# Kernel optimization log

Hardware: AMD Instinct MI355X
Metric: run time of the kernel (lower is better)

Reference implementation:

```python
import jax, jax.numpy as jnp
import numpy as np

SHAPES = ((64, 64), (32, 32), (16, 16), (8, 8))
LEVEL_STARTS = np.concatenate([[0], np.cumsum([h * w for h, w in SHAPES])]).tolist()
N_LEVELS = 4; N_HEADS = 8; N_POINTS = 4; D_MODEL = 256; HEAD_DIM = 32; D_FFN = 1024; NUM_LAYERS = 2
LEN_IN = sum(h * w for h, w in SHAPES)
BATCH = 2


def setup_inputs():
    key = jax.random.key(0)
    ks = iter(jax.random.split(key, 40))
    r = lambda shape, s=1.0: jax.random.normal(next(ks), shape, dtype=jnp.float32) * s
    L = NUM_LAYERS
    return {
        "src": r((BATCH, LEN_IN, D_MODEL)),
        "pos": r((BATCH, LEN_IN, D_MODEL), 0.5),
        "valid_ratios": jnp.ones((BATCH, N_LEVELS, 2), jnp.float32),
        "Wv": r((L, D_MODEL, D_MODEL), 0.05), "bv": jnp.zeros((L, D_MODEL), jnp.float32),
        "Woff": r((L, D_MODEL, N_HEADS * N_LEVELS * N_POINTS * 2), 0.002),
        "boff": r((L, N_HEADS * N_LEVELS * N_POINTS * 2), 0.5),
        "Wa": r((L, D_MODEL, N_HEADS * N_LEVELS * N_POINTS), 0.05),
        "ba": jnp.zeros((L, N_HEADS * N_LEVELS * N_POINTS), jnp.float32),
        "Wo": r((L, D_MODEL, D_MODEL), 0.05), "bo": jnp.zeros((L, D_MODEL), jnp.float32),
        "g1": jnp.ones((L, D_MODEL), jnp.float32), "be1": jnp.zeros((L, D_MODEL), jnp.float32),
        "Wl1": r((L, D_MODEL, D_FFN), 0.05), "bl1": jnp.zeros((L, D_FFN), jnp.float32),
        "Wl2": r((L, D_FFN, D_MODEL), 0.05), "bl2": jnp.zeros((L, D_MODEL), jnp.float32),
        "g2": jnp.ones((L, D_MODEL), jnp.float32), "be2": jnp.zeros((L, D_MODEL), jnp.float32),
    }


def layer_norm(x, g, b, eps=1e-5):
    m = jnp.mean(x, -1, keepdims=True)
    v = jnp.mean(jnp.square(x - m), -1, keepdims=True)
    return (x - m) * jax.lax.rsqrt(v + eps) * g + b


def make_reference_points(valid_ratios):
    # DeformableTransformerEncoder.get_reference_points, vectorized per level
    refs = []
    for lvl, (H, W) in enumerate(SHAPES):
        gy, gx = jnp.meshgrid(jnp.arange(H, dtype=jnp.float32) + 0.5,
                              jnp.arange(W, dtype=jnp.float32) + 0.5, indexing="ij")
        ry = gy.reshape(-1)[None] / (valid_ratios[:, lvl, 1][:, None] * H)
        rx = gx.reshape(-1)[None] / (valid_ratios[:, lvl, 0][:, None] * W)
        refs.append(jnp.stack([rx, ry], -1))  # [N, H*W, 2]
    ref = jnp.concatenate(refs, 1)  # [N, Len, 2]
    return ref[:, :, None, :] * valid_ratios[:, None]  # [N, Len, n_levels, 2]


def ms_deform_attn(query, input_flatten, reference_points, Wv, bv, Woff, boff, Wa, ba, Wo, bo):
    N, Lq, _ = query.shape
    value = (input_flatten @ Wv + bv).reshape(N, -1, N_HEADS, HEAD_DIM)
    off = (query @ Woff + boff).reshape(N, Lq, N_HEADS, N_LEVELS, N_POINTS, 2)
    aw = (query @ Wa + ba).reshape(N, Lq, N_HEADS, N_LEVELS * N_POINTS)
    aw = jax.nn.softmax(aw, -1).reshape(N, Lq, N_HEADS, N_LEVELS, N_POINTS)
    # normalizer is (W, H) per level, as in MSDeformAttn
    normalizer = jnp.array([[w, h] for h, w in SHAPES], jnp.float32)
    loc = reference_points[:, :, None, :, None, :] + off / normalizer[None, None, None, :, None, :]
    acc = jnp.zeros((N, N_HEADS, Lq, HEAD_DIM), query.dtype)
    for lvl, (H, W) in enumerate(SHAPES):
        s = LEVEL_STARTS[lvl]
        val = value[:, s:s + H * W].transpose(0, 2, 1, 3)  # [N, heads, H*W, hd]
        # grid_sample bilinear, align_corners=False, zero padding
        x = loc[:, :, :, lvl, :, 0] * W - 0.5  # [N, Lq, heads, P]
        y = loc[:, :, :, lvl, :, 1] * H - 0.5
        x0 = jnp.floor(x); y0 = jnp.floor(y)
        wx1 = x - x0; wy1 = y - y0
        ix0 = x0.astype(jnp.int32); iy0 = y0.astype(jnp.int32)

        def corner(ix, iy, w):
            valid = (ix >= 0) & (ix < W) & (iy >= 0) & (iy < H)
            idx = jnp.clip(iy, 0, H - 1) * W + jnp.clip(ix, 0, W - 1)
            idx = idx.transpose(0, 2, 1, 3).reshape(N, N_HEADS, Lq * N_POINTS)
            g = jnp.take_along_axis(val, idx[..., None], axis=2).reshape(N, N_HEADS, Lq, N_POINTS, HEAD_DIM)
            w = jnp.where(valid, w, 0.0).transpose(0, 2, 1, 3)  # [N, heads, Lq, P]
            return g * w[..., None]

        sampled = (corner(ix0, iy0, (1 - wx1) * (1 - wy1))
                   + corner(ix0 + 1, iy0, wx1 * (1 - wy1))
                   + corner(ix0, iy0 + 1, (1 - wx1) * wy1)
                   + corner(ix0 + 1, iy0 + 1, wx1 * wy1))
        acc = acc + (sampled * aw[:, :, :, lvl].transpose(0, 2, 1, 3)[..., None]).sum(3)
    out = acc.transpose(0, 2, 1, 3).reshape(N, Lq, D_MODEL)
    return out @ Wo + bo


def reference(src, pos, valid_ratios, Wv, bv, Woff, boff, Wa, ba, Wo, bo,
              g1, be1, Wl1, bl1, Wl2, bl2, g2, be2):
    ref_pts = make_reference_points(valid_ratios)
    out = src
    for l in range(NUM_LAYERS):
        q = out + pos  # with_pos_embed
        attn = ms_deform_attn(q, out, ref_pts, Wv[l], bv[l], Woff[l], boff[l],
                              Wa[l], ba[l], Wo[l], bo[l])
        out = layer_norm(out + attn, g1[l], be1[l])
        ffn = jax.nn.relu(out @ Wl1[l] + bl1[l]) @ Wl2[l] + bl2[l]
        out = layer_norm(out + ffn, g2[l], be2[l])
    return out
```

## Files before the change

### kernel.cpp

```cpp
#include <hip/hip_runtime.h>
#include <math.h>

#define LEN   5440
#define NB    2
#define MROWS (NB * LEN)
#define DM    256
#define NH    8
#define HD    32
#define NLV   4
#define NPT   4
#define DFFN  1024

typedef __attribute__((ext_vector_type(8))) short bf16x8;
typedef __attribute__((ext_vector_type(4))) short bf16x4;
typedef __attribute__((ext_vector_type(4))) float f32x4;

#define MFMA16 __builtin_amdgcn_mfma_f32_16x16x32_bf16

__device__ __forceinline__ short f2bf(float f) {
    union { float f; unsigned u; } cv; cv.f = f;
    unsigned r = cv.u + 0x7fffu + ((cv.u >> 16) & 1u);
    return (short)(r >> 16);
}
__device__ __forceinline__ float bf2f(short s) {
    union { unsigned u; float f; } cv;
    cv.u = ((unsigned)(unsigned short)s) << 16;
    return cv.f;
}

__device__ __forceinline__ void gload16(const short* g, short* l) {
    __builtin_amdgcn_global_load_lds(
        (__attribute__((address_space(1))) void*)g,
        (__attribute__((address_space(3))) void*)l, 16, 0, 0);
}

template <int N> __device__ __forceinline__ void vmwait();
template <> __device__ __forceinline__ void vmwait<0>() { asm volatile("s_waitcnt vmcnt(0)" ::: "memory"); }
template <> __device__ __forceinline__ void vmwait<4>() { asm volatile("s_waitcnt vmcnt(4)" ::: "memory"); }
template <> __device__ __forceinline__ void vmwait<5>() { asm volatile("s_waitcnt vmcnt(5)" ::: "memory"); }

__device__ __forceinline__ int swz(int row) { return (row >> 1) & 3; }

__global__ __launch_bounds__(256) void prep_all(
    const float* __restrict__ Wv,  const float* __restrict__ Woff,
    const float* __restrict__ Wa,  const float* __restrict__ Wo,
    const float* __restrict__ Wl1, const float* __restrict__ Wl2,
    short* __restrict__ out,
    const float4* __restrict__ s4, const float4* __restrict__ p4,
    bf16x4* __restrict__ curb, bf16x4* __restrict__ qb)
{
    __shared__ short T[32][33];
    if (blockIdx.x >= 1472) {
        const int i = (blockIdx.x - 1472) * 256 + threadIdx.x;
        float4 s = s4[i], p = p4[i];
        bf16x4 c, q;
        c[0] = f2bf(s.x); c[1] = f2bf(s.y); c[2] = f2bf(s.z); c[3] = f2bf(s.w);
        q[0] = f2bf(s.x + p.x); q[1] = f2bf(s.y + p.y);
        q[2] = f2bf(s.z + p.z); q[3] = f2bf(s.w + p.w);
        curb[i] = c; qb[i] = q;
        return;
    }
    int bx = blockIdx.x;
    int l  = bx / 736;
    int t  = bx % 736;
    const float* src; int K, N; long doff;
    if      (t < 64)  { src = Wv;   K = 256;  N = 256;  doff = 0;      }
    else if (t < 128) { src = Woff; K = 256;  N = 256;  doff = 65536;  t -= 64;  }
    else if (t < 160) { src = Wa;   K = 256;  N = 128;  doff = 131072; t -= 128; }
    else if (t < 224) { src = Wo;   K = 256;  N = 256;  doff = 163840; t -= 160; }
    else if (t < 480) { src = Wl1;  K = 256;  N = 1024; doff = 229376; t -= 224; }
    else              { src = Wl2;  K = 1024; N = 256;  doff = 491520; t -= 480; }
    src += (long)l * K * N;
    short* dst = out + (long)l * 753664 + doff;

    const int ntx = N / 32;
    const int n0 = (t % ntx) * 32, k0 = (t / ntx) * 32;

    const int tid = threadIdx.x;
    {
        const int n = tid & 31, kq = tid >> 5;
        #pragma unroll
        for (int i = 0; i < 4; ++i) {
            int k = kq * 4 + i;
            T[n][k] = f2bf(src[(long)(k0 + k) * N + n0 + n]);
        }
    }
    __syncthreads();
    {
        const int k = tid & 31, nq = tid >> 5;
        #pragma unroll
        for (int i = 0; i < 4; ++i) {
            int n = nq * 4 + i;
            dst[(long)(n0 + n) * K + k0 + k] = T[n][k];
        }
    }
}

template <int RELU, int OMODE, int K>
__device__ __forceinline__ void gemm_core128_v2(
    short* As, short* Bs,
    const short* __restrict__ A, const short* __restrict__ Wt,
    const float* __restrict__ bias, float* __restrict__ Cf,
    short* __restrict__ Cb, int ldc, int m0, int wrow0, int ccol0)
{
    constexpr int NT = K / 32;
    static_assert(NT >= 4 && (NT & 1) == 0, "NT even >= 4");
    const int t    = threadIdx.x;
    const int wave = t >> 6, lane = t & 63;
    const int wm   = (wave & 1) * 64;
    const int wn   = (wave >> 1) * 64;
    const int lm   = lane & 15;
    const int chkg = lane >> 4;

    const short* aS[2]; const short* bS[2];
    short *aD[2], *bD[2];
    #pragma unroll
    for (int i = 0; i < 2; ++i) {
        const int c   = wave * 2 + i;
        const int row = c * 16 + (lane >> 2);
        const int xc  = (lane & 3) ^ swz(row);
        aS[i] = A  + (long)(m0 + row) * K + xc * 8;
        bS[i] = Wt + (long)(wrow0 + row) * K + xc * 8;
        aD[i] = As + c * 512;
        bD[i] = Bs + c * 512;
    }

    int offA[4], offB[4];
    #pragma unroll
    for (int s = 0; s < 4; ++s) {
        const int r = wm + s * 16 + lm;
        offA[s] = r * 32 + (chkg ^ swz(r)) * 8;
    }
    #pragma unroll
    for (int u = 0; u < 4; ++u) {
        const int r = wn + u * 16 + lm;
        offB[u] = r * 32 + (chkg ^ swz(r)) * 8;
    }

    f32x4 acc[4][4] = {};

#define STG128(BUF, KT) do {                                          \
        const int _ko = (KT) * 32;                                    \
        gload16(aS[0] + _ko, aD[0] + (BUF) * 4096);                   \
        gload16(bS[0] + _ko, bD[0] + (BUF) * 4096);                   \
        gload16(aS[1] + _ko, aD[1] + (BUF) * 4096);                   \
        gload16(bS[1] + _ko, bD[1] + (BUF) * 4096);                   \
    } while (0)

#define GB128(T, BUF, WN, DOSTAGE) do {                               \
        vmwait<WN>();                                                 \
        __builtin_amdgcn_s_barrier();                                 \
        bf16x8 af[4], bv[4];                                          \
        _Pragma("unroll")                                             \
        for (int s = 0; s < 4; ++s)                                   \
            af[s] = *(const bf16x8*)(As + (BUF) * 4096 + offA[s]);    \
        _Pragma("unroll")                                             \
        for (int u = 0; u < 4; ++u)                                   \
            bv[u] = *(const bf16x8*)(Bs + (BUF) * 4096 + offB[u]);    \
        asm volatile("s_waitcnt lgkmcnt(0)" ::: "memory");            \
        __builtin_amdgcn_s_barrier();                                 \
        __builtin_amdgcn_sched_barrier(0);                            \
        if (DOSTAGE) STG128(BUF, (T) + 2);                            \
        _Pragma("unroll")                                             \
        for (int s = 0; s < 4; ++s)                                   \
            _Pragma("unroll")                                         \
            for (int u = 0; u < 4; ++u)                               \
                acc[s][u] = MFMA16(af[s], bv[u], acc[s][u], 0, 0, 0); \
    } while (0)

    STG128(0, 0);
    STG128(1, 1);
    for (int tt = 0; tt < NT - 2; tt += 2) {
        GB128(tt,     0, 4, true);
        GB128(tt + 1, 1, 4, true);
    }
    GB128(NT - 2, 0, 4, false);
    GB128(NT - 1, 1, 0, false);
#undef GB128
#undef STG128

    const int col = lane & 15;
    const int rq  = (lane >> 4) * 4;
    #pragma unroll
    for (int s = 0; s < 4; ++s) {
        #pragma unroll
        for (int u = 0; u < 4; ++u) {
            const int gn = ccol0 + wn + u * 16 + col;
            const float bb = bias[gn];
            #pragma unroll
            for (int r = 0; r < 4; ++r) {
                const int gm = m0 + wm + s * 16 + rq + r;
                float v = acc[s][u][r] + bb;
                if (RELU) v = fmaxf(v, 0.f);
                if (OMODE == 0) {
                    Cf[(long)gm * ldc + gn] = v;
                } else if (OMODE == 1) {
                    Cb[(long)gm * ldc + gn] = f2bf(v);
                } else {
                    const int n   = gm / LEN;
                    const int pix = gm - n * LEN;
                    const int h   = gn >> 5, d = gn & 31;
                    Cb[((long)(n * NH + h) * LEN + pix) * 32 + d] = f2bf(v);
                }
            }
        }
    }
}

template <int RELU, int OMODE, int K>
__global__ __launch_bounds__(256) void gemm128v2(
    const short* __restrict__ A, const short* __restrict__ Wt,
    const float* __restrict__ bias, float* Cf, short* Cb, int ldc)
{
    __shared__ __align__(16) short As[2 * 128 * 32];
    __shared__ __align__(16) short Bs[2 * 128 * 32];
    gemm_core128_v2<RELU, OMODE, K>(As, Bs, A, Wt, bias, Cf, Cb, ldc,
                                    blockIdx.y * 128, blockIdx.x * 128,
                                    blockIdx.x * 128);
}

__global__ __launch_bounds__(256) void gemm_qkv128(
    const short* __restrict__ curb, const short* __restrict__ qb,
    const short* __restrict__ Wt, const float* __restrict__ bv,
    const float* __restrict__ boff, const float* __restrict__ ba,
    short* __restrict__ Vb, float* __restrict__ OFF, float* __restrict__ AW)
{
    __shared__ __align__(16) short As[2 * 128 * 32];
    __shared__ __align__(16) short Bs[2 * 128 * 32];
    const int n0 = blockIdx.x * 128;
    if (n0 < 256) {
        gemm_core128_v2<0, 2, 256>(As, Bs, curb, Wt, bv, (float*)nullptr, Vb,
                                   256, blockIdx.y * 128, n0, n0);
    } else if (n0 < 512) {
        gemm_core128_v2<0, 0, 256>(As, Bs, qb, Wt, boff, OFF, (short*)nullptr,
                                   256, blockIdx.y * 128, n0, n0 - 256);
    } else {
        gemm_core128_v2<0, 0, 256>(As, Bs, qb, Wt, ba, AW, (short*)nullptr,
                                   128, blockIdx.y * 128, n0, n0 - 512);
    }
}

template <int K>
__global__ __launch_bounds__(256) void gemm_ln(
    const short* __restrict__ A, const short* __restrict__ Wt,
    const float* __restrict__ bias, const short* __restrict__ residb,
    const float* __restrict__ g, const float* __restrict__ be,
    short* __restrict__ outb, short* __restrict__ outq,
    float* __restrict__ outf, const float* __restrict__ pos)
{
    constexpr int NT = K / 32;
    __shared__ __align__(16) short As[2 * 32 * 32];
    __shared__ __align__(16) short Bs[2 * 256 * 32];
    __shared__ float red[2][32][2];

    const int t    = threadIdx.x;
    const int wave = t >> 6, lane = t & 63;
    const int wm   = (wave & 1) * 16;
    const int wn   = (wave >> 1) * 128;
    const int lm   = lane & 15;
    const int chkg = lane >> 4;
    const int rq   = chkg * 4;
    const int m0   = blockIdx.x * 32;
    const bool hasA = (wave & 1) == 0;

    short rr[8][4];
    #pragma unroll
    for (int u = 0; u < 8; ++u)
        #pragma unroll
        for (int r = 0; r < 4; ++r)
            rr[u][r] = residb[(long)(m0 + wm + rq + r) * DM + wn + u * 16 + lm];
    asm volatile("" ::: "memory");

    const short* bSp[4]; short* bDp[4];
    #pragma unroll
    for (int i = 0; i < 4; ++i) {
        const int c   = wave * 4 + i;
        const int row = c * 16 + (lane >> 2);
        const int xc  = (lane & 3) ^ swz(row);
        bSp[i] = Wt + (long)row * K + xc * 8;
        bDp[i] = Bs + c * 512;
    }
    const short* aSp = nullptr; short* aDp = nullptr;
    if (hasA) {
        const int c   = wave >> 1;
        const int row = c * 16 + (lane >> 2);
        const int xc  = (lane & 3) ^ swz(row);
        aSp = A + (long)(m0 + row) * K + xc * 8;
        aDp = As + c * 512;
    }

    const int offA = (wm + lm) * 32 + (chkg ^ swz(wm + lm)) * 8;
    int offB[8];
    #pragma unroll
    for (int u = 0; u < 8; ++u) {
        const int r = wn + u * 16 + lm;
        offB[u] = r * 32 + (chkg ^ swz(r)) * 8;
    }

    f32x4 acc[8] = {};

#define STGL(BUF, KT) do {                                            \
        const int _ko = (KT) * 32;                                    \
        if (hasA) gload16(aSp + _ko, aDp + (BUF) * 1024);             \
        gload16(bSp[0] + _ko, bDp[0] + (BUF) * 8192);                 \
        gload16(bSp[1] + _ko, bDp[1] + (BUF) * 8192);                 \
        gload16(bSp[2] + _ko, bDp[2] + (BUF) * 8192);                 \
        gload16(bSp[3] + _ko, bDp[3] + (BUF) * 8192);                 \
    } while (0)

#define GBLN(T, BUF, WA, WB, DOSTAGE) do {                            \
        if (hasA) vmwait<WA>(); else vmwait<WB>();                    \
        __builtin_amdgcn_s_barrier();                                 \
        bf16x8 af = *(const bf16x8*)(As + (BUF) * 1024 + offA);       \
        bf16x8 bv[8];                                                 \
        _Pragma("unroll")                                             \
        for (int u = 0; u < 8; ++u)                                   \
            bv[u] = *(const bf16x8*)(Bs + (BUF) * 8192 + offB[u]);    \
        asm volatile("s_waitcnt lgkmcnt(0)" ::: "memory");            \
        __builtin_amdgcn_s_barrier();                                 \
        __builtin_amdgcn_sched_barrier(0);                            \
        if (DOSTAGE) STGL(BUF, (T) + 2);                              \
        _Pragma("unroll")                                             \
        for (int u = 0; u < 8; ++u)                                   \
            acc[u] = MFMA16(af, bv[u], acc[u], 0, 0, 0);              \
    } while (0)

    STGL(0, 0);
    STGL(1, 1);
    for (int tt = 0; tt < NT - 2; tt += 2) {
        GBLN(tt,     0, 5, 4, true);
        GBLN(tt + 1, 1, 5, 4, true);
    }
    GBLN(NT - 2, 0, 5, 4, false);
    GBLN(NT - 1, 1, 0, 0, false);
#undef GBLN
#undef STGL

    #pragma unroll
    for (int u = 0; u < 8; ++u) {
        const int gn = wn + u * 16 + lm;
        const float bb = bias[gn];
        #pragma unroll
        for (int r = 0; r < 4; ++r)
            acc[u][r] += bb + bf2f(rr[u][r]);
    }

    float rs[4], r2[4];
    #pragma unroll
    for (int r = 0; r < 4; ++r) {
        float s = 0.f, s2 = 0.f;
        #pragma unroll
        for (int u = 0; u < 8; ++u) { const float v = acc[u][r]; s += v; s2 += v * v; }
        rs[r] = s; r2[r] = s2;
    }
    #pragma unroll
    for (int o = 1; o < 16; o <<= 1)
        #pragma unroll
        for (int r = 0; r < 4; ++r) {
            rs[r] += __shfl_xor(rs[r], o, 64);
            r2[r] += __shfl_xor(r2[r], o, 64);
        }
    if (lm == 0) {
        #pragma unroll
        for (int r = 0; r < 4; ++r) {
            red[wave >> 1][wm + rq + r][0] = rs[r];
            red[wave >> 1][wm + rq + r][1] = r2[r];
        }
    }
    __syncthreads();
    #pragma unroll
    for (int r = 0; r < 4; ++r) {
        const int row = wm + rq + r;
        const float ts = red[0][row][0] + red[1][row][0];
        const float t2 = red[0][row][1] + red[1][row][1];
        const float mean = ts * (1.f / DM);
        const float var  = t2 * (1.f / DM) - mean * mean;
        rs[r] = mean;
        r2[r] = rsqrtf(var + 1e-5f);
    }
    #pragma unroll
    for (int u = 0; u < 8; ++u) {
        const int gn = wn + u * 16 + lm;
        const float gg = g[gn], bbe = be[gn];
        #pragma unroll
        for (int r = 0; r < 4; ++r) {
            const long gm = m0 + wm + rq + r;
            const float o = (acc[u][r] - rs[r]) * r2[r] * gg + bbe;
            if (outb) outb[gm * DM + gn] = f2bf(o);
            if (outq) outq[gm * DM + gn] = f2bf(o + pos[gm * DM + gn]);
            if (outf) outf[gm * DM + gn] = o;
        }
    }
}

template <int KLEN, int KSTR>
__global__ __launch_bounds__(256) void ln2_part_k(
    const short* __restrict__ A0, const short* __restrict__ Wt0,
    float* __restrict__ PART)
{
    constexpr int NT = KLEN / 32;
    static_assert(NT >= 4 && (NT & 1) == 0, "NT even >= 4");
    __shared__ __align__(16) short As[2 * 32 * 32];
    __shared__ __align__(16) short Bs[2 * 256 * 32];

    const int kk = blockIdx.x;
    const int m0 = blockIdx.y * 32;
    const short* A  = A0  + kk * KLEN;
    const short* Wt = Wt0 + kk * KLEN;
    float* Pout = PART + (long)kk * MROWS * DM;

    const int t    = threadIdx.x;
    const int wave = t >> 6, lane = t & 63;
    const int wm   = (wave & 1) * 16;
    const int wn   = (wave >> 1) * 128;
    const int lm   = lane & 15;
    const int chkg = lane >> 4;
    const int rq   = chkg * 4;
    const bool hasA = (wave & 1) == 0;

    const short* bSp[4]; short* bDp[4];
    #pragma unroll
    for (int i = 0; i < 4; ++i) {
        const int c   = wave * 4 + i;
        const int row = c * 16 + (lane >> 2);
        const int xc  = (lane & 3) ^ swz(row);
        bSp[i] = Wt + (long)row * KSTR + xc * 8;
        bDp[i] = Bs + c * 512;
    }
    const short* aSp = nullptr; short* aDp = nullptr;
    if (hasA) {
        const int c   = wave >> 1;
        const int row = c * 16 + (lane >> 2);
        const int xc  = (lane & 3) ^ swz(row);
        aSp = A + (long)(m0 + row) * KSTR + xc * 8;
        aDp = As + c * 512;
    }

    const int offA = (wm + lm) * 32 + (chkg ^ swz(wm + lm)) * 8;
    int offB[8];
    #pragma unroll
    for (int u = 0; u < 8; ++u) {
        const int r = wn + u * 16 + lm;
        offB[u] = r * 32 + (chkg ^ swz(r)) * 8;
    }

    f32x4 acc[8] = {};

#define STGP(BUF, KT) do {                                            \
        const int _ko = (KT) * 32;                                    \
        if (hasA) gload16(aSp + _ko, aDp + (BUF) * 1024);             \
        gload16(bSp[0] + _ko, bDp[0] + (BUF) * 8192);                 \
        gload16(bSp[1] + _ko, bDp[1] + (BUF) * 8192);                 \
        gload16(bSp[2] + _ko, bDp[2] + (BUF) * 8192);                 \
        gload16(bSp[3] + _ko, bDp[3] + (BUF) * 8192);                 \
    } while (0)

#define GBP(T, BUF, WA, WB, DOSTAGE) do {                             \
        if (hasA) vmwait<WA>(); else vmwait<WB>();                    \
        __builtin_amdgcn_s_barrier();                                 \
        bf16x8 af = *(const bf16x8*)(As + (BUF) * 1024 + offA);       \
        bf16x8 bv[8];                                                 \
        _Pragma("unroll")                                             \
        for (int u = 0; u < 8; ++u)                                   \
            bv[u] = *(const bf16x8*)(Bs + (BUF) * 8192 + offB[u]);    \
        asm volatile("s_waitcnt lgkmcnt(0)" ::: "memory");            \
        __builtin_amdgcn_s_barrier();                                 \
        __builtin_amdgcn_sched_barrier(0);                            \
        if (DOSTAGE) STGP(BUF, (T) + 2);                              \
        _Pragma("unroll")                                             \
        for (int u = 0; u < 8; ++u)                                   \
            acc[u] = MFMA16(af, bv[u], acc[u], 0, 0, 0);              \
    } while (0)

    STGP(0, 0);
    STGP(1, 1);
    for (int tt = 0; tt < NT - 2; tt += 2) {
        GBP(tt,     0, 5, 4, true);
        GBP(tt + 1, 1, 5, 4, true);
    }
    GBP(NT - 2, 0, 5, 4, false);
    GBP(NT - 1, 1, 0, 0, false);
#undef GBP
#undef STGP

    #pragma unroll
    for (int u = 0; u < 8; ++u) {
        const int gn = wn + u * 16 + lm;
        #pragma unroll
        for (int r = 0; r < 4; ++r)
            Pout[(long)(m0 + wm + rq + r) * DM + gn] = acc[u][r];
    }
}

__global__ __launch_bounds__(256) void ln2_fin_k(
    const float* __restrict__ PART, const short* __restrict__ residb,
    const float* __restrict__ bl2, const float* __restrict__ g,
    const float* __restrict__ be, short* __restrict__ outb,
    short* __restrict__ outq, float* __restrict__ outf,
    const float* __restrict__ pos)
{
    const int wave = threadIdx.x >> 6, lane = threadIdx.x & 63;
    const int c0 = lane * 4;
    const f32x4 bb = *(const f32x4*)(bl2 + c0);
    const f32x4 gg = *(const f32x4*)(g + c0);
    const f32x4 ee = *(const f32x4*)(be + c0);
    #pragma unroll 1
    for (int r = 0; r < 8; ++r) {
        const long row = (long)blockIdx.x * 32 + wave * 8 + r;
        const f32x4 p0 = *(const f32x4*)(PART + row * DM + c0);
        const f32x4 p1 = *(const f32x4*)(PART + (long)MROWS * DM + row * DM + c0);
        const bf16x4 rr = *(const bf16x4*)(residb + row * DM + c0);
        float v[4]; float s = 0.f, s2 = 0.f;
        #pragma unroll
        for (int j = 0; j < 4; ++j) {
            v[j] = p0[j] + p1[j] + bb[j] + bf2f(rr[j]);
            s += v[j]; s2 += v[j] * v[j];
        }
        #pragma unroll
        for (int o = 1; o < 64; o <<= 1) {
            s  += __shfl_xor(s,  o, 64);
            s2 += __shfl_xor(s2, o, 64);
        }
        const float mean = s * (1.f / DM);
        const float var  = s2 * (1.f / DM) - mean * mean;
        const float rstd = rsqrtf(var + 1e-5f);
        float o4[4];
        #pragma unroll
        for (int j = 0; j < 4; ++j)
            o4[j] = (v[j] - mean) * rstd * gg[j] + ee[j];
        if (outb) {
            bf16x4 ob;
            #pragma unroll
            for (int j = 0; j < 4; ++j) ob[j] = f2bf(o4[j]);
            *(bf16x4*)(outb + row * DM + c0) = ob;
        }
        if (outq) {
            const f32x4 pp = *(const f32x4*)(pos + row * DM + c0);
            bf16x4 oq;
            #pragma unroll
            for (int j = 0; j < 4; ++j) oq[j] = f2bf(o4[j] + pp[j]);
            *(bf16x4*)(outq + row * DM + c0) = oq;
        }
        if (outf) {
            f32x4 of;
            #pragma unroll
            for (int j = 0; j < 4; ++j) of[j] = o4[j];
            *(f32x4*)(outf + row * DM + c0) = of;
        }
    }
}

__global__ __launch_bounds__(256) void deform_attn_v3(
    const short* __restrict__ Vb,
    const float* __restrict__ OFF,
    const float* __restrict__ AW,
    const float* __restrict__ vr,
    bf16x4* __restrict__ ATTb)
{
    const int starts[5] = {0, 4096, 5120, 5376, 5440};
    const int dims[4]   = {64, 32, 16, 8};

    const int wave = threadIdx.x >> 6;
    const int lane = threadIdx.x & 63;
    const int h    = lane >> 3;
    const int d4   = lane & 7;

    const int gq = blockIdx.x * 4 + wave;
    const int n  = gq / LEN;
    const int q  = gq % LEN;

    int lq = 3;
    if (q < 4096) lq = 0; else if (q < 5120) lq = 1; else if (q < 5376) lq = 2;
    const int r  = q - starts[lq];
    const int Wq = dims[lq];
    const int gy = r / Wq, gx = r % Wq;
    const float vrxq = vr[(n * NLV + lq) * 2 + 0];
    const float vryq = vr[(n * NLV + lq) * 2 + 1];
    const float rx = (gx + 0.5f) / (vrxq * Wq);
    const float ry = (gy + 0.5f) / (vryq * Wq);

    const long row = (long)n * LEN + q;

    const float* awp = AW + row * 128 + h * 16;
    float a[16];
    float mx = -1e30f;
    #pragma unroll
    for (int i = 0; i < 16; ++i) { a[i] = awp[i]; mx = fmaxf(mx, a[i]); }
    float s = 0.f;
    #pragma unroll
    for (int i = 0; i < 16; ++i) { a[i] = __expf(a[i] - mx); s += a[i]; }
    const float inv = 1.f / s;

    const float* offp = OFF + row * 256 + h * 32;

    float4 acc = {0.f, 0.f, 0.f, 0.f};
    #pragma unroll
    for (int lvl = 0; lvl < NLV; ++lvl) {
        const int Hl = dims[lvl];
        const int Wl = Hl;
        const float fW = (float)Wl;
        const int sb = starts[lvl];
        const float lx = rx * vr[(n * NLV + lvl) * 2 + 0];
        const float ly = ry * vr[(n * NLV + lvl) * 2 + 1];
        const short* vb = Vb + ((long)(n * NH + h) * LEN + sb) * 32 + d4 * 4;
        #pragma unroll
        for (int p = 0; p < NPT; ++p) {
            const float ox = offp[lvl * 8 + p * 2 + 0];
            const float oy = offp[lvl * 8 + p * 2 + 1];
            const float x = fmaf(lx, fW, ox) - 0.5f;
            const float y = fmaf(ly, fW, oy) - 0.5f;
            const float x0f = floorf(x), y0f = floorf(y);
            const int ix0 = (int)x0f, iy0 = (int)y0f;
            const float wx1 = x - x0f, wy1 = y - y0f;
            const float wx0 = 1.f - wx1, wy0 = 1.f - wy1;

            const bool vx0 = (ix0 >= 0)     && (ix0 < Wl);
            const bool vx1 = (ix0 + 1 >= 0) && (ix0 + 1 < Wl);
            const bool vy0 = (iy0 >= 0)     && (iy0 < Hl);
            const bool vy1 = (iy0 + 1 >= 0) && (iy0 + 1 < Hl);
            const int cx0 = min(max(ix0, 0), Wl - 1);
            const int cx1 = min(max(ix0 + 1, 0), Wl - 1);
            const int cy0 = min(max(iy0, 0), Hl - 1);
            const int cy1 = min(max(iy0 + 1, 0), Hl - 1);

            const float w00 = (vx0 && vy0) ? wx0 * wy0 : 0.f;
            const float w10 = (vx1 && vy0) ? wx1 * wy0 : 0.f;
            const float w01 = (vx0 && vy1) ? wx0 * wy1 : 0.f;
            const float w11 = (vx1 && vy1) ? wx1 * wy1 : 0.f;

            const bf16x4 g00 = *(const bf16x4*)(vb + (long)(cy0 * Wl + cx0) * 32);
            const bf16x4 g10 = *(const bf16x4*)(vb + (long)(cy0 * Wl + cx1) * 32);
            const bf16x4 g01 = *(const bf16x4*)(vb + (long)(cy1 * Wl + cx0) * 32);
            const bf16x4 g11 = *(const bf16x4*)(vb + (long)(cy1 * Wl + cx1) * 32);

            const float awv = a[lvl * 4 + p] * inv;
            #pragma unroll
            for (int e = 0; e < 4; ++e) {
                float sv = w00 * bf2f(g00[e]) + w10 * bf2f(g10[e])
                         + w01 * bf2f(g01[e]) + w11 * bf2f(g11[e]);
                (&acc.x)[e] += awv * sv;
            }
        }
    }
    bf16x4 ob;
    ob[0] = f2bf(acc.x); ob[1] = f2bf(acc.y);
    ob[2] = f2bf(acc.z); ob[3] = f2bf(acc.w);
    ATTb[row * 64 + h * 8 + d4] = ob;
}

extern "C" void kernel_launch(void* const* d_in, const int* in_sizes, int n_in,
                              void* d_out, int out_size, void* d_ws, size_t ws_size,
                              hipStream_t stream)
{
    const float* src = (const float*)d_in[0];
    const float* pos = (const float*)d_in[1];
    const float* vr  = (const float*)d_in[2];
    const float* Wv_   = (const float*)d_in[3];
    const float* bv_   = (const float*)d_in[4];
    const float* Woff_ = (const float*)d_in[5];
    const float* boff_ = (const float*)d_in[6];
    const float* Wa_   = (const float*)d_in[7];
    const float* ba_   = (const float*)d_in[8];
    const float* Wo_   = (const float*)d_in[9];
    const float* bo_   = (const float*)d_in[10];
    const float* g1_   = (const float*)d_in[11];
    const float* be1_  = (const float*)d_in[12];
    const float* Wl1_  = (const float*)d_in[13];
    const float* bl1_  = (const float*)d_in[14];
    const float* Wl2_  = (const float*)d_in[15];
    const float* bl2_  = (const float*)d_in[16];
    const float* g2_   = (const float*)d_in[17];
    const float* be2_  = (const float*)d_in[18];

    const long SZ = (long)MROWS * DM;
    float* ws = (float*)d_ws;
    float* OFF  = ws;
    float* AW   = OFF + SZ;
    short* Vb   = (short*)(AW + (long)MROWS * 128);
    short* curb = Vb   + SZ;
    short* qb   = curb + SZ;
    short* ATTb = qb   + SZ;
    short* XAb  = ATTb + SZ;
    short* FFNb = XAb  + SZ;
    short* Wt   = FFNb + (long)MROWS * DFFN;
    float* PART = (float*)(Wt + 2L * 753664);

    const dim3 blk(256);
    const int GYM = MROWS / 128;
    const int GLN = MROWS / 32;

    hipLaunchKernelGGL(prep_all, dim3(1472 + SZ / 4 / 256), blk, 0, stream,
                       Wv_, Woff_, Wa_, Wo_, Wl1_, Wl2_, Wt,
                       (const float4*)src, (const float4*)pos,
                       (bf16x4*)curb, (bf16x4*)qb);

    for (int l = 0; l < 2; ++l) {
        const short* Wbase = Wt + (long)l * 753664;
        const float* bv   = bv_   + (long)l * DM;
        const float* boff = boff_ + (long)l * 256;
        const float* ba   = ba_   + (long)l * 128;
        const float* bo   = bo_   + (long)l * DM;
        const float* g1   = g1_   + (long)l * DM;
        const float* be1  = be1_  + (long)l * DM;
        const float* bl1  = bl1_  + (long)l * DFFN;
        const float* bl2  = bl2_  + (long)l * DM;
        const float* g2   = g2_   + (long)l * DM;
        const float* be2  = be2_  + (long)l * DM;

        hipLaunchKernelGGL(gemm_qkv128, dim3(5, GYM), blk, 0, stream,
                           curb, qb, Wbase, bv, boff, ba, Vb, OFF, AW);
        hipLaunchKernelGGL(deform_attn_v3, dim3(MROWS / 4), blk, 0, stream,
                           Vb, OFF, AW, vr, (bf16x4*)ATTb);
        hipLaunchKernelGGL((gemm_ln<256>), dim3(GLN), blk, 0, stream,
                           ATTb, Wbase + 163840, bo, curb, g1, be1,
                           XAb, (short*)nullptr, (float*)nullptr,
                           (const float*)nullptr);
        hipLaunchKernelGGL((gemm128v2<1, 1, 256>), dim3(8, GYM), blk, 0, stream,
                           XAb, Wbase + 229376, bl1, (float*)nullptr, FFNb, 1024);
        hipLaunchKernelGGL((ln2_part_k<512, 1024>), dim3(2, GLN), blk, 0, stream,
                           FFNb, Wbase + 491520, PART);
        if (l == 0) {
            hipLaunchKernelGGL(ln2_fin_k, dim3(GLN), blk, 0, stream,
                               PART, XAb, bl2, g2, be2,
                               curb, qb, (float*)nullptr, pos);
        } else {
            hipLaunchKernelGGL(ln2_fin_k, dim3(GLN), blk, 0, stream,
                               PART, XAb, bl2, g2, be2,
                               (short*)nullptr, (short*)nullptr,
                               (float*)d_out, (const float*)nullptr);
        }
    }
}
```

Baseline: 293.8 us.

## Double GEMM K-tile depth to 64 with 8-way XOR swizzled LDS layout

All bf16 MFMA GEMM kernels (QKV, FFN1, output-proj+LN, FFN2 partial) now stage 64-wide K tiles instead of 32, halving the number of barrier/wait iterations and issuing two MFMAs per fragment per step. The LDS layout changes to 64-element rows with a row&7 XOR swizzle, and the per-wave load distribution is reworked so all waves load A uniformly. LDS use doubles per block (up to ~72KB for the LN kernels), which may reduce occupancy; the static_assert NT>=4 now requires K>=256, which the K=256 GEMMs exactly meet.

```diff
diff --git a/kernel.cpp b/kernel.cpp
--- a/kernel.cpp
+++ b/kernel.cpp
@@ -36,10 +36,9 @@
 
 template <int N> __device__ __forceinline__ void vmwait();
 template <> __device__ __forceinline__ void vmwait<0>() { asm volatile("s_waitcnt vmcnt(0)" ::: "memory"); }
-template <> __device__ __forceinline__ void vmwait<4>() { asm volatile("s_waitcnt vmcnt(4)" ::: "memory"); }
-template <> __device__ __forceinline__ void vmwait<5>() { asm volatile("s_waitcnt vmcnt(5)" ::: "memory"); }
-
-__device__ __forceinline__ int swz(int row) { return (row >> 1) & 3; }
+template <> __device__ __forceinline__ void vmwait<8>() { asm volatile("s_waitcnt vmcnt(8)" ::: "memory"); }
+template <> __device__ __forceinline__ void vmwait<9>() { asm volatile("s_waitcnt vmcnt(9)" ::: "memory"); }
+
 
 __global__ __launch_bounds__(256) void prep_all(
     const float* __restrict__ Wv,  const float* __restrict__ Woff,
@@ -97,13 +96,13 @@
 }
 
 template <int RELU, int OMODE, int K>
-__device__ __forceinline__ void gemm_core128_v2(
+__device__ __forceinline__ void gemm_core128_v3(
     short* As, short* Bs,
     const short* __restrict__ A, const short* __restrict__ Wt,
     const float* __restrict__ bias, float* __restrict__ Cf,
     short* __restrict__ Cb, int ldc, int m0, int wrow0, int ccol0)
 {
-    constexpr int NT = K / 32;
+    constexpr int NT = K / 64;
     static_assert(NT >= 4 && (NT & 1) == 0, "NT even >= 4");
     const int t    = threadIdx.x;
     const int wave = t >> 6, lane = t & 63;
@@ -112,72 +111,78 @@
     const int lm   = lane & 15;
     const int chkg = lane >> 4;
 
-    const short* aS[2]; const short* bS[2];
-    short *aD[2], *bD[2];
-    #pragma unroll
-    for (int i = 0; i < 2; ++i) {
-        const int c   = wave * 2 + i;
-        const int row = c * 16 + (lane >> 2);
-        const int xc  = (lane & 3) ^ swz(row);
-        aS[i] = A  + (long)(m0 + row) * K + xc * 8;
-        bS[i] = Wt + (long)(wrow0 + row) * K + xc * 8;
-        aD[i] = As + c * 512;
-        bD[i] = Bs + c * 512;
+    const short* aS[4]; const short* bS[4];
+    int ldst[4];
+    #pragma unroll
+    for (int j = 0; j < 4; ++j) {
+        const int row = wave * 32 + j * 8 + (lane >> 3);
+        const int sc  = (lane & 7) ^ (row & 7);
+        aS[j] = A  + (long)(m0 + row) * K + sc * 8;
+        bS[j] = Wt + (long)(wrow0 + row) * K + sc * 8;
+        ldst[j] = wave * 2048 + j * 512;
     }
 
     int offA[4], offB[4];
     #pragma unroll
     for (int s = 0; s < 4; ++s) {
         const int r = wm + s * 16 + lm;
-        offA[s] = r * 32 + (chkg ^ swz(r)) * 8;
+        offA[s] = r * 64 + ((chkg ^ (r & 7)) * 8);
     }
     #pragma unroll
     for (int u = 0; u < 4; ++u) {
         const int r = wn + u * 16 + lm;
-        offB[u] = r * 32 + (chkg ^ swz(r)) * 8;
+        offB[u] = r * 64 + ((chkg ^ (r & 7)) * 8);
     }
 
     f32x4 acc[4][4] = {};
 
-#define STG128(BUF, KT) do {                                          \
-        const int _ko = (KT) * 32;                                    \
-        gload16(aS[0] + _ko, aD[0] + (BUF) * 4096);                   \
-        gload16(bS[0] + _ko, bD[0] + (BUF) * 4096);                   \
-        gload16(aS[1] + _ko, aD[1] + (BUF) * 4096);                   \
-        gload16(bS[1] + _ko, bD[1] + (BUF) * 4096);                   \
+#define STG3(BUF, KT) do {                                            \
+        const int _ko = (KT) * 64;                                    \
+        _Pragma("unroll")                                             \
+        for (int j = 0; j < 4; ++j)                                   \
+            gload16(aS[j] + _ko, As + (BUF) * 8192 + ldst[j]);        \
+        _Pragma("unroll")                                             \
+        for (int j = 0; j < 4; ++j)                                   \
+            gload16(bS[j] + _ko, Bs + (BUF) * 8192 + ldst[j]);        \
     } while (0)
 
-#define GB128(T, BUF, WN, DOSTAGE) do {                               \
+#define GB3(T, BUF, WN, DOSTAGE) do {                                 \
         vmwait<WN>();                                                 \
         __builtin_amdgcn_s_barrier();                                 \
-        bf16x8 af[4], bv[4];                                          \
-        _Pragma("unroll")                                             \
-        for (int s = 0; s < 4; ++s)                                   \
-            af[s] = *(const bf16x8*)(As + (BUF) * 4096 + offA[s]);    \
-        _Pragma("unroll")                                             \
-        for (int u = 0; u < 4; ++u)                                   \
-            bv[u] = *(const bf16x8*)(Bs + (BUF) * 4096 + offB[u]);    \
+        bf16x8 a0[4], a1[4], b0[4], b1[4];                            \
+        _Pragma("unroll")                                             \
+        for (int s = 0; s < 4; ++s) {                                 \
+            a0[s] = *(const bf16x8*)(As + (BUF) * 8192 + offA[s]);    \
+            a1[s] = *(const bf16x8*)(As + (BUF) * 8192 + (offA[s] ^ 32)); \
+        }                                                             \
+        _Pragma("unroll")                                             \
+        for (int u = 0; u < 4; ++u) {                                 \
+            b0[u] = *(const bf16x8*)(Bs + (BUF) * 8192 + offB[u]);    \
+            b1[u] = *(const bf16x8*)(Bs + (BUF) * 8192 + (offB[u] ^ 32)); \
+        }                                                             \
         asm volatile("s_waitcnt lgkmcnt(0)" ::: "memory");            \
         __builtin_amdgcn_s_barrier();                                 \
         __builtin_amdgcn_sched_barrier(0);                            \
-        if (DOSTAGE) STG128(BUF, (T) + 2);                            \
+        if (DOSTAGE) STG3(BUF, (T) + 2);                              \
         _Pragma("unroll")                                             \
         for (int s = 0; s < 4; ++s)                                   \
             _Pragma("unroll")                                         \
-            for (int u = 0; u < 4; ++u)                               \
-                acc[s][u] = MFMA16(af[s], bv[u], acc[s][u], 0, 0, 0); \
+            for (int u = 0; u < 4; ++u) {                             \
+                acc[s][u] = MFMA16(a0[s], b0[u], acc[s][u], 0, 0, 0); \
+                acc[s][u] = MFMA16(a1[s], b1[u], acc[s][u], 0, 0, 0); \
+            }                                                         \
     } while (0)
 
-    STG128(0, 0);
-    STG128(1, 1);
+    STG3(0, 0);
+    STG3(1, 1);
     for (int tt = 0; tt < NT - 2; tt += 2) {
-        GB128(tt,     0, 4, true);
-        GB128(tt + 1, 1, 4, true);
-    }
-    GB128(NT - 2, 0, 4, false);
-    GB128(NT - 1, 1, 0, false);
-#undef GB128
-#undef STG128
+        GB3(tt,     0, 8, true);
+        GB3(tt + 1, 1, 8, true);
+    }
+    GB3(NT - 2, 0, 8, false);
+    GB3(NT - 1, 1, 0, false);
+#undef GB3
+#undef STG3
 
     const int col = lane & 15;
     const int rq  = (lane >> 4) * 4;
@@ -208,13 +213,13 @@
 }
 
 template <int RELU, int OMODE, int K>
-__global__ __launch_bounds__(256) void gemm128v2(
+__global__ __launch_bounds__(256) void gemm128v3(
     const short* __restrict__ A, const short* __restrict__ Wt,
     const float* __restrict__ bias, float* Cf, short* Cb, int ldc)
 {
-    __shared__ __align__(16) short As[2 * 128 * 32];
-    __shared__ __align__(16) short Bs[2 * 128 * 32];
-    gemm_core128_v2<RELU, OMODE, K>(As, Bs, A, Wt, bias, Cf, Cb, ldc,
+    __shared__ __align__(16) short As[2 * 128 * 64];
+    __shared__ __align__(16) short Bs[2 * 128 * 64];
+    gemm_core128_v3<RELU, OMODE, K>(As, Bs, A, Wt, bias, Cf, Cb, ldc,
                                     blockIdx.y * 128, blockIdx.x * 128,
                                     blockIdx.x * 128);
 }
@@ -225,17 +230,17 @@
     const float* __restrict__ boff, const float* __restrict__ ba,
     short* __restrict__ Vb, float* __restrict__ OFF, float* __restrict__ AW)
 {
-    __shared__ __align__(16) short As[2 * 128 * 32];
-    __shared__ __align__(16) short Bs[2 * 128 * 32];
+    __shared__ __align__(16) short As[2 * 128 * 64];
+    __shared__ __align__(16) short Bs[2 * 128 * 64];
     const int n0 = blockIdx.x * 128;
     if (n0 < 256) {
-        gemm_core128_v2<0, 2, 256>(As, Bs, curb, Wt, bv, (float*)nullptr, Vb,
+        gemm_core128_v3<0, 2, 256>(As, Bs, curb, Wt, bv, (float*)nullptr, Vb,
                                    256, blockIdx.y * 128, n0, n0);
     } else if (n0 < 512) {
-        gemm_core128_v2<0, 0, 256>(As, Bs, qb, Wt, boff, OFF, (short*)nullptr,
+        gemm_core128_v3<0, 0, 256>(As, Bs, qb, Wt, boff, OFF, (short*)nullptr,
                                    256, blockIdx.y * 128, n0, n0 - 256);
     } else {
-        gemm_core128_v2<0, 0, 256>(As, Bs, qb, Wt, ba, AW, (short*)nullptr,
+        gemm_core128_v3<0, 0, 256>(As, Bs, qb, Wt, ba, AW, (short*)nullptr,
                                    128, blockIdx.y * 128, n0, n0 - 512);
     }
 }
@@ -248,9 +253,10 @@
     short* __restrict__ outb, short* __restrict__ outq,
     float* __restrict__ outf, const float* __restrict__ pos)
 {
-    constexpr int NT = K / 32;
-    __shared__ __align__(16) short As[2 * 32 * 32];
-    __shared__ __align__(16) short Bs[2 * 256 * 32];
+    constexpr int NT = K / 64;
+    static_assert(NT >= 4 && (NT & 1) == 0, "NT even >= 4");
+    __shared__ __align__(16) short As[2 * 32 * 64];
+    __shared__ __align__(16) short Bs[2 * 256 * 64];
     __shared__ float red[2][32][2];
 
     const int t    = threadIdx.x;
@@ -261,7 +267,6 @@
     const int chkg = lane >> 4;
     const int rq   = chkg * 4;
     const int m0   = blockIdx.x * 32;
-    const bool hasA = (wave & 1) == 0;
 
     short rr[8][4];
     #pragma unroll
@@ -271,68 +276,66 @@
             rr[u][r] = residb[(long)(m0 + wm + rq + r) * DM + wn + u * 16 + lm];
     asm volatile("" ::: "memory");
 
-    const short* bSp[4]; short* bDp[4];
-    #pragma unroll
-    for (int i = 0; i < 4; ++i) {
-        const int c   = wave * 4 + i;
-        const int row = c * 16 + (lane >> 2);
-        const int xc  = (lane & 3) ^ swz(row);
-        bSp[i] = Wt + (long)row * K + xc * 8;
-        bDp[i] = Bs + c * 512;
-    }
-    const short* aSp = nullptr; short* aDp = nullptr;
-    if (hasA) {
-        const int c   = wave >> 1;
-        const int row = c * 16 + (lane >> 2);
-        const int xc  = (lane & 3) ^ swz(row);
-        aSp = A + (long)(m0 + row) * K + xc * 8;
-        aDp = As + c * 512;
-    }
-
-    const int offA = (wm + lm) * 32 + (chkg ^ swz(wm + lm)) * 8;
+    const int arow = t >> 3;
+    const short* aSp = A + (long)(m0 + arow) * K + (((t & 7) ^ (arow & 7)) * 8);
+    const int aDst = wave * 512;
+    const short* bSp[8]; int bDst[8];
+    #pragma unroll
+    for (int j = 0; j < 8; ++j) {
+        const int row = wave * 64 + j * 8 + (lane >> 3);
+        const int sc  = (lane & 7) ^ (row & 7);
+        bSp[j] = Wt + (long)row * K + sc * 8;
+        bDst[j] = wave * 4096 + j * 512;
+    }
+
+    const int offA = (wm + lm) * 64 + ((chkg ^ ((wm + lm) & 7)) * 8);
     int offB[8];
     #pragma unroll
     for (int u = 0; u < 8; ++u) {
         const int r = wn + u * 16 + lm;
-        offB[u] = r * 32 + (chkg ^ swz(r)) * 8;
+        offB[u] = r * 64 + ((chkg ^ (r & 7)) * 8);
     }
 
     f32x4 acc[8] = {};
 
 #define STGL(BUF, KT) do {                                            \
-        const int _ko = (KT) * 32;                                    \
-        if (hasA) gload16(aSp + _ko, aDp + (BUF) * 1024);             \
-        gload16(bSp[0] + _ko, bDp[0] + (BUF) * 8192);                 \
-        gload16(bSp[1] + _ko, bDp[1] + (BUF) * 8192);                 \
-        gload16(bSp[2] + _ko, bDp[2] + (BUF) * 8192);                 \
-        gload16(bSp[3] + _ko, bDp[3] + (BUF) * 8192);                 \
+        const int _ko = (KT) * 64;                                    \
+        gload16(aSp + _ko, As + (BUF) * 2048 + aDst);                 \
+        _Pragma("unroll")                                             \
+        for (int j = 0; j < 8; ++j)                                   \
+            gload16(bSp[j] + _ko, Bs + (BUF) * 16384 + bDst[j]);      \
     } while (0)
 
-#define GBLN(T, BUF, WA, WB, DOSTAGE) do {                            \
-        if (hasA) vmwait<WA>(); else vmwait<WB>();                    \
+#define GBLN(T, BUF, WN, DOSTAGE) do {                                \
+        vmwait<WN>();                                                 \
         __builtin_amdgcn_s_barrier();                                 \
-        bf16x8 af = *(const bf16x8*)(As + (BUF) * 1024 + offA);       \
-        bf16x8 bv[8];                                                 \
-        _Pragma("unroll")                                             \
-        for (int u = 0; u < 8; ++u)                                   \
-            bv[u] = *(const bf16x8*)(Bs + (BUF) * 8192 + offB[u]);    \
+        bf16x8 af0 = *(const bf16x8*)(As + (BUF) * 2048 + offA);      \
+        bf16x8 af1 = *(const bf16x8*)(As + (BUF) * 2048 + (offA ^ 32)); \
+        bf16x8 b0[8], b1[8];                                          \
+        _Pragma("unroll")                                             \
+        for (int u = 0; u < 8; ++u) {                                 \
+            b0[u] = *(const bf16x8*)(Bs + (BUF) * 16384 + offB[u]);   \
+            b1[u] = *(const bf16x8*)(Bs + (BUF) * 16384 + (offB[u] ^ 32)); \
+        }                                                             \
         asm volatile("s_waitcnt lgkmcnt(0)" ::: "memory");            \
         __builtin_amdgcn_s_barrier();                                 \
         __builtin_amdgcn_sched_barrier(0);                            \
         if (DOSTAGE) STGL(BUF, (T) + 2);                              \
         _Pragma("unroll")                                             \
-        for (int u = 0; u < 8; ++u)                                   \
-            acc[u] = MFMA16(af, bv[u], acc[u], 0, 0, 0);              \
+        for (int u = 0; u < 8; ++u) {                                 \
+            acc[u] = MFMA16(af0, b0[u], acc[u], 0, 0, 0);             \
+            acc[u] = MFMA16(af1, b1[u], acc[u], 0, 0, 0);             \
+        }                                                             \
     } while (0)
 
     STGL(0, 0);
     STGL(1, 1);
     for (int tt = 0; tt < NT - 2; tt += 2) {
-        GBLN(tt,     0, 5, 4, true);
-        GBLN(tt + 1, 1, 5, 4, true);
-    }
-    GBLN(NT - 2, 0, 5, 4, false);
-    GBLN(NT - 1, 1, 0, 0, false);
+        GBLN(tt,     0, 9, true);
+        GBLN(tt + 1, 1, 9, true);
+    }
+    GBLN(NT - 2, 0, 9, false);
+    GBLN(NT - 1, 1, 0, false);
 #undef GBLN
 #undef STGL
 
@@ -398,10 +401,10 @@
     const short* __restrict__ A0, const short* __restrict__ Wt0,
     float* __restrict__ PART)
 {
-    constexpr int NT = KLEN / 32;
+    constexpr int NT = KLEN / 64;
     static_assert(NT >= 4 && (NT & 1) == 0, "NT even >= 4");
-    __shared__ __align__(16) short As[2 * 32 * 32];
-    __shared__ __align__(16) short Bs[2 * 256 * 32];
+    __shared__ __align__(16) short As[2 * 32 * 64];
+    __shared__ __align__(16) short Bs[2 * 256 * 64];
 
     const int kk = blockIdx.x;
     const int m0 = blockIdx.y * 32;
@@ -416,70 +419,67 @@
     const int lm   = lane & 15;
     const int chkg = lane >> 4;
     const int rq   = chkg * 4;
-    const bool hasA = (wave & 1) == 0;
-
-    const short* bSp[4]; short* bDp[4];
-    #pragma unroll
-    for (int i = 0; i < 4; ++i) {
-        const int c   = wave * 4 + i;
-        const int row = c * 16 + (lane >> 2);
-        const int xc  = (lane & 3) ^ swz(row);
-        bSp[i] = Wt + (long)row * KSTR + xc * 8;
-        bDp[i] = Bs + c * 512;
-    }
-    const short* aSp = nullptr; short* aDp = nullptr;
-    if (hasA) {
-        const int c   = wave >> 1;
-        const int row = c * 16 + (lane >> 2);
-        const int xc  = (lane & 3) ^ swz(row);
-        aSp = A + (long)(m0 + row) * KSTR + xc * 8;
-        aDp = As + c * 512;
-    }
-
-    const int offA = (wm + lm) * 32 + (chkg ^ swz(wm + lm)) * 8;
+
+    const int arow = t >> 3;
+    const short* aSp = A + (long)(m0 + arow) * KSTR + (((t & 7) ^ (arow & 7)) * 8);
+    const int aDst = wave * 512;
+    const short* bSp[8]; int bDst[8];
+    #pragma unroll
+    for (int j = 0; j < 8; ++j) {
+        const int row = wave * 64 + j * 8 + (lane >> 3);
+        const int sc  = (lane & 7) ^ (row & 7);
+        bSp[j] = Wt + (long)row * KSTR + sc * 8;
+        bDst[j] = wave * 4096 + j * 512;
+    }
+
+    const int offA = (wm + lm) * 64 + ((chkg ^ ((wm + lm) & 7)) * 8);
     int offB[8];
     #pragma unroll
     for (int u = 0; u < 8; ++u) {
         const int r = wn + u * 16 + lm;
-        offB[u] = r * 32 + (chkg ^ swz(r)) * 8;
+        offB[u] = r * 64 + ((chkg ^ (r & 7)) * 8);
     }
 
     f32x4 acc[8] = {};
 
 #define STGP(BUF, KT) do {                                            \
-        const int _ko = (KT) * 32;                                    \
-        if (hasA) gload16(aSp + _ko, aDp + (BUF) * 1024);             \
-        gload16(bSp[0] + _ko, bDp[0] + (BUF) * 8192);                 \
-        gload16(bSp[1] + _ko, bDp[1] + (BUF) * 8192);                 \
-        gload16(bSp[2] + _ko, bDp[2] + (BUF) * 8192);                 \
-        gload16(bSp[3] + _ko, bDp[3] + (BUF) * 8192);                 \
+        const int _ko = (KT) * 64;                                    \
+        gload16(aSp + _ko, As + (BUF) * 2048 + aDst);                 \
+        _Pragma("unroll")                                             \
+        for (int j = 0; j < 8; ++j)                                   \
+            gload16(bSp[j] + _ko, Bs + (BUF) * 16384 + bDst[j]);      \
     } while (0)
 
-#define GBP(T, BUF, WA, WB, DOSTAGE) do {                             \
-        if (hasA) vmwait<WA>(); else vmwait<WB>();                    \
+#define GBP(T, BUF, WN, DOSTAGE) do {                                 \
+        vmwait<WN>();                                                 \
         __builtin_amdgcn_s_barrier();                                 \
-        bf16x8 af = *(const bf16x8*)(As + (BUF) * 1024 + offA);       \
-        bf16x8 bv[8];                                                 \
-        _Pragma("unroll")                                             \
-        for (int u = 0; u < 8; ++u)                                   \
-            bv[u] = *(const bf16x8*)(Bs + (BUF) * 8192 + offB[u]);    \
+        bf16x8 af0 = *(const bf16x8*)(As + (BUF) * 2048 + offA);      \
+        bf16x8 af1 = *(const bf16x8*)(As + (BUF) * 2048 + (offA ^ 32)); \
+        bf16x8 b0[8], b1[8];                                          \
+        _Pragma("unroll")                                             \
+        for (int u = 0; u < 8; ++u) {                                 \
+            b0[u] = *(const bf16x8*)(Bs + (BUF) * 16384 + offB[u]);   \
+            b1[u] = *(const bf16x8*)(Bs + (BUF) * 16384 + (offB[u] ^ 32)); \
+        }                                                             \
         asm volatile("s_waitcnt lgkmcnt(0)" ::: "memory");            \
         __builtin_amdgcn_s_barrier();                                 \
         __builtin_amdgcn_sched_barrier(0);                            \
         if (DOSTAGE) STGP(BUF, (T) + 2);                              \
         _Pragma("unroll")                                             \
-        for (int u = 0; u < 8; ++u)                                   \
-            acc[u] = MFMA16(af, bv[u], acc[u], 0, 0, 0);              \
+        for (int u = 0; u < 8; ++u) {                                 \
+            acc[u] = MFMA16(af0, b0[u], acc[u], 0, 0, 0);             \
+            acc[u] = MFMA16(af1, b1[u], acc[u], 0, 0, 0);             \
+        }                                                             \
     } while (0)
 
     STGP(0, 0);
     STGP(1, 1);
     for (int tt = 0; tt < NT - 2; tt += 2) {
-        GBP(tt,     0, 5, 4, true);
-        GBP(tt + 1, 1, 5, 4, true);
-    }
-    GBP(NT - 2, 0, 5, 4, false);
-    GBP(NT - 1, 1, 0, 0, false);
+        GBP(tt,     0, 9, true);
+        GBP(tt + 1, 1, 9, true);
+    }
+    GBP(NT - 2, 0, 9, false);
+    GBP(NT - 1, 1, 0, false);
 #undef GBP
 #undef STGP
 
@@ -715,7 +715,7 @@
                            ATTb, Wbase + 163840, bo, curb, g1, be1,
                            XAb, (short*)nullptr, (float*)nullptr,
                            (const float*)nullptr);
-        hipLaunchKernelGGL((gemm128v2<1, 1, 256>), dim3(8, GYM), blk, 0, stream,
+        hipLaunchKernelGGL((gemm128v3<1, 1, 256>), dim3(8, GYM), blk, 0, stream,
                            XAb, Wbase + 229376, bl1, (float*)nullptr, FFNb, 1024);
         hipLaunchKernelGGL((ln2_part_k<512, 1024>), dim3(2, GLN), blk, 0, stream,
                            FFNb, Wbase + 491520, PART);
```

Measured after the change: 287.6 us. 1.02x faster.
